# Kernel tuning notes

Measured on AMD Instinct MI355X. Metric: run time of the kernel, lower is better.

The kernel has to match this reference:

```python
import jax, jax.numpy as jnp
import numpy as np

T, D, N, K, H, F = 2048, 4096, 32, 8, 128, 14336
THETA = 500000.0
EPS = 1e-5


def setup_inputs() -> dict:
    key = jax.random.key(0)
    ks = jax.random.split(key, 10)
    s = 0.02  # weight init scale
    return {
        "x": jax.random.normal(ks[0], (T, D), jnp.float32),
        "positions": jnp.arange(T, dtype=jnp.int32),
        "ln1_scale": jnp.ones((D,), jnp.float32),
        "w_q": jax.random.normal(ks[1], (D, N, H), jnp.float32) * s,
        "w_k": jax.random.normal(ks[2], (D, K, H), jnp.float32) * s,
        "w_v": jax.random.normal(ks[3], (D, K, H), jnp.float32) * s,
        "w_o": jax.random.normal(ks[4], (N, H, D), jnp.float32) * s,
        "ln2_scale": jnp.ones((D,), jnp.float32),
        "w_gate": jax.random.normal(ks[5], (D, F), jnp.float32) * s,
        "w_up": jax.random.normal(ks[6], (D, F), jnp.float32) * s,
        "w_down": jax.random.normal(ks[7], (F, D), jnp.float32) * s,
    }


def _rms_norm(x, scale):
    var = jnp.mean(jnp.square(x), axis=-1, keepdims=True)
    return x * jax.lax.rsqrt(var + EPS) * scale


def _apply_rope(x, pos):
    # x: [T, heads, H]; Llama rotate-half RoPE
    half = H // 2
    inv_freq = 1.0 / (THETA ** (jnp.arange(half, dtype=jnp.float32) / half))
    ang = pos.astype(jnp.float32)[:, None] * inv_freq[None, :]      # [T, half]
    cos = jnp.cos(ang)[:, None, :]
    sin = jnp.sin(ang)[:, None, :]
    x1, x2 = x[..., :half], x[..., half:]
    return jnp.concatenate([x1 * cos - x2 * sin, x2 * cos + x1 * sin], axis=-1)


def reference(x, positions, ln1_scale, w_q, w_k, w_v, w_o, ln2_scale, w_gate, w_up, w_down):
    # --- input RMSNorm ---
    h = _rms_norm(x, ln1_scale)
    # --- QKV projections + RoPE ---
    q = _apply_rope(jnp.einsum('td,dnh->tnh', h, w_q), positions)   # [T,N,H]
    k = _apply_rope(jnp.einsum('td,dkh->tkh', h, w_k), positions)   # [T,K,H]
    v = jnp.einsum('td,dkh->tkh', h, w_v)                            # [T,K,H]
    # --- GQA causal attention (prefill) ---
    G = N // K
    qg = q.reshape(T, K, G, H)
    scale = 1.0 / jnp.sqrt(jnp.float32(H))
    scores = jnp.einsum('tkgh,skh->kgts', qg, k) * scale             # [K,G,T,T]
    causal = positions[:, None] >= positions[None, :]                # [T,T]
    scores = jnp.where(causal[None, None], scores, jnp.finfo(scores.dtype).min)
    probs = jax.nn.softmax(scores, axis=-1)
    attn = jnp.einsum('kgts,skh->tkgh', probs, v).reshape(T, N, H)
    attn_out = jnp.einsum('tnh,nhd->td', attn, w_o)
    # --- residual ---
    residual = attn_out + x
    # --- post-attn RMSNorm + SwiGLU MLP ---
    h2 = _rms_norm(residual, ln2_scale)
    gate = jax.nn.silu(h2 @ w_gate)
    up = h2 @ w_up
    out = (gate * up) @ w_down
    return residual + out
```

## Files before the change

kernel.cpp:

```cpp
#include <hip/hip_runtime.h>

typedef __attribute__((ext_vector_type(8))) short bf16x8;
typedef __attribute__((ext_vector_type(4))) float f32x4;

constexpr int T = 2048;
constexpr int D = 4096;
constexpr int NQ = 32;
constexpr int NKV = 8;
constexpr int H = 128;
constexpr int F = 14336;
constexpr int NQKV = (NQ + 2 * NKV) * H;
constexpr int VOFF = (NQ + NKV) * H;

__device__ inline unsigned short f2bf(float f) {
  unsigned u = __float_as_uint(f);
  return (unsigned short)((u + 0x7FFFu + ((u >> 16) & 1u)) >> 16);
}

__device__ inline void gload_lds16(const void* g, void* l) {
  __builtin_amdgcn_global_load_lds((const __attribute__((address_space(1))) void*)g,
                                   (__attribute__((address_space(3))) void*)l, 16, 0, 0);
}

#define MFMA16(a, b, c) __builtin_amdgcn_mfma_f32_16x16x32_bf16(a, b, c, 0, 0, 0)

template <int MODE>
__global__ __launch_bounds__(256) void transpose_bf16(const float* __restrict__ in,
                                                      unsigned short* __restrict__ out,
                                                      int K, int N) {
  __shared__ float tile[64 * 65];
  const int kb = blockIdx.x * 64;
  const int nb = blockIdx.y * 64;
  const int tid = threadIdx.x;
  const int r = tid >> 2;
  const int c4 = tid & 3;
#pragma unroll
  for (int i = 0; i < 4; ++i) {
    float4 v = *(const float4*)(in + (size_t)(kb + r) * N + nb + c4 * 16 + i * 4);
    *(float4*)&tile[r * 65 + c4 * 16 + i * 4] = v;
  }
  __syncthreads();
  const int n = tid >> 2;
  const int kq = tid & 3;
  int nsrc = nb + n;
  int prow = (MODE == 0) ? nsrc : ((nsrc >> 4) * 32 + (nsrc & 15) + (MODE == 2 ? 16 : 0));
#pragma unroll
  for (int half = 0; half < 2; ++half) {
    ushort4 o0, o1;
    int k0 = kq * 16 + half * 8;
    o0.x = f2bf(tile[(k0 + 0) * 65 + n]);
    o0.y = f2bf(tile[(k0 + 1) * 65 + n]);
    o0.z = f2bf(tile[(k0 + 2) * 65 + n]);
    o0.w = f2bf(tile[(k0 + 3) * 65 + n]);
    o1.x = f2bf(tile[(k0 + 4) * 65 + n]);
    o1.y = f2bf(tile[(k0 + 5) * 65 + n]);
    o1.z = f2bf(tile[(k0 + 6) * 65 + n]);
    o1.w = f2bf(tile[(k0 + 7) * 65 + n]);
    unsigned short* op = out + (size_t)prow * K + kb + k0;
    *(ushort4*)(op + 0) = o0;
    *(ushort4*)(op + 4) = o1;
  }
}

__global__ __launch_bounds__(256) void rmsnorm_kernel(
    const float* __restrict__ in, const float* __restrict__ scale,
    unsigned short* __restrict__ out) {
  int row = blockIdx.x;
  const float4* xr = (const float4*)(in + (size_t)row * D);
  const float4* sr = (const float4*)scale;
  float4 vals[4];
  float ss = 0.f;
#pragma unroll
  for (int i = 0; i < 4; ++i) {
    float4 v = xr[threadIdx.x + i * 256];
    vals[i] = v;
    ss += v.x * v.x + v.y * v.y + v.z * v.z + v.w * v.w;
  }
#pragma unroll
  for (int off = 32; off; off >>= 1) ss += __shfl_xor(ss, off, 64);
  __shared__ float wsum[4];
  if ((threadIdx.x & 63) == 0) wsum[threadIdx.x >> 6] = ss;
  __syncthreads();
  float r = rsqrtf((wsum[0] + wsum[1] + wsum[2] + wsum[3]) * (1.f / D) + 1e-5f);
#pragma unroll
  for (int i = 0; i < 4; ++i) {
    int vi = threadIdx.x + i * 256;
    float4 v = vals[i];
    float4 s = sr[vi];
    ushort4 o;
    o.x = f2bf(v.x * r * s.x);
    o.y = f2bf(v.y * r * s.y);
    o.z = f2bf(v.z * r * s.z);
    o.w = f2bf(v.w * r * s.w);
    *(ushort4*)(out + (size_t)row * D + (size_t)vi * 4) = o;
  }
}

__global__ __launch_bounds__(256) void rmsnorm_add3(
    const float* __restrict__ a, const float* __restrict__ b,
    const float* __restrict__ c, const float* __restrict__ scale,
    float* __restrict__ residOut, unsigned short* __restrict__ out) {
  int row = blockIdx.x;
  const float4* ar = (const float4*)(a + (size_t)row * D);
  const float4* br = (const float4*)(b + (size_t)row * D);
  const float4* cr = (const float4*)(c + (size_t)row * D);
  const float4* sr = (const float4*)scale;
  float4* rr = (float4*)(residOut + (size_t)row * D);
  float4 vals[4];
  float ss = 0.f;
#pragma unroll
  for (int i = 0; i < 4; ++i) {
    int vi = threadIdx.x + i * 256;
    float4 va = ar[vi], vb = br[vi], vc = cr[vi];
    float4 v;
    v.x = va.x + vb.x + vc.x;
    v.y = va.y + vb.y + vc.y;
    v.z = va.z + vb.z + vc.z;
    v.w = va.w + vb.w + vc.w;
    vals[i] = v;
    ss += v.x * v.x + v.y * v.y + v.z * v.z + v.w * v.w;
  }
#pragma unroll
  for (int off = 32; off; off >>= 1) ss += __shfl_xor(ss, off, 64);
  __shared__ float wsum[4];
  if ((threadIdx.x & 63) == 0) wsum[threadIdx.x >> 6] = ss;
  __syncthreads();
  float r = rsqrtf((wsum[0] + wsum[1] + wsum[2] + wsum[3]) * (1.f / D) + 1e-5f);
#pragma unroll
  for (int i = 0; i < 4; ++i) {
    int vi = threadIdx.x + i * 256;
    float4 v = vals[i];
    rr[vi] = v;
    float4 s = sr[vi];
    ushort4 o;
    o.x = f2bf(v.x * r * s.x);
    o.y = f2bf(v.y * r * s.y);
    o.z = f2bf(v.z * r * s.z);
    o.w = f2bf(v.w * r * s.w);
    *(ushort4*)(out + (size_t)row * D + (size_t)vi * 4) = o;
  }
}

__global__ __launch_bounds__(256) void add3_kernel(const float* __restrict__ a,
                                                   const float* __restrict__ b,
                                                   const float* __restrict__ c,
                                                   float* __restrict__ o) {
  int i = blockIdx.x * 256 + threadIdx.x;
  float4 va = ((const float4*)a)[i];
  float4 vb = ((const float4*)b)[i];
  float4 vc = ((const float4*)c)[i];
  float4 vo;
  vo.x = va.x + vb.x + vc.x;
  vo.y = va.y + vb.y + vc.y;
  vo.z = va.z + vb.z + vc.z;
  vo.w = va.w + vb.w + vc.w;
  ((float4*)o)[i] = vo;
}

__global__ __launch_bounds__(256) void rope_table(const int* __restrict__ pos,
                                                  float* __restrict__ ctab,
                                                  float* __restrict__ stab) {
  int idx = blockIdx.x * 256 + threadIdx.x;
  int t = idx >> 6, i = idx & 63;
  float inv = exp2f(-(float)i * (log2f(500000.0f) / 64.0f));
  float ang = (float)pos[t] * inv;
  ctab[idx] = cosf(ang);
  stab[idx] = sinf(ang);
}

__global__ __launch_bounds__(256) void rope_bf16(const float* __restrict__ x,
                                                 const float* __restrict__ ctab,
                                                 const float* __restrict__ stab,
                                                 unsigned short* __restrict__ out,
                                                 int nheads, int row_stride, float scale) {
  int idx = blockIdx.x * 256 + threadIdx.x;
  int i = idx & 63;
  int tn = idx >> 6;
  int t = tn / nheads;
  int n = tn - t * nheads;
  float c = ctab[t * 64 + i], s = stab[t * 64 + i];
  const float* p = x + (size_t)t * row_stride + n * H;
  float x1 = p[i], x2 = p[i + 64];
  unsigned short* o = out + (size_t)tn * H;
  o[i] = f2bf((x1 * c - x2 * s) * scale);
  o[i + 64] = f2bf((x2 * c + x1 * s) * scale);
}

template <int EP>
__global__ __launch_bounds__(256) void gemm_bf(
    const unsigned short* __restrict__ A, const unsigned short* __restrict__ Bt0,
    float* __restrict__ outF, unsigned short* __restrict__ outB, int Kd, int Nd) {
  __shared__ unsigned short lA[128 * 32];
  __shared__ unsigned short lB0[128 * 32];

  const int tid = threadIdx.x;
  const int m0 = blockIdx.x * 128;
  const int n0 = blockIdx.y * 128;
  const int lane = tid & 63;
  const int wv = tid >> 6;

  f32x4 acc[4][4];
#pragma unroll
  for (int i = 0; i < 4; ++i)
#pragma unroll
    for (int j = 0; j < 4; ++j) acc[i][j] = (f32x4){0.f, 0.f, 0.f, 0.f};

  const int wr = (wv >> 1) * 64;
  const int wc = (wv & 1) * 64;
  const int k8 = (lane >> 4) * 8;
  const int rl = lane & 15;
  const int sidx0 = wv * 512 + lane * 8;

  for (int k0 = 0; k0 < Kd; k0 += 32) {
    __syncthreads();
#pragma unroll
    for (int it = 0; it < 2; ++it) {
      int idx = sidx0 + it * 2048;
      int row = idx >> 5, kk = idx & 31;
      int base = wv * 512 + it * 2048;
      gload_lds16(A + (size_t)(m0 + row) * Kd + k0 + kk, &lA[base]);
      gload_lds16(Bt0 + (size_t)(n0 + row) * Kd + k0 + kk, &lB0[base]);
    }
    asm volatile("s_waitcnt vmcnt(0)" ::: "memory");
    __syncthreads();

    bf16x8 af[4], bfr[4];
#pragma unroll
    for (int i = 0; i < 4; ++i)
      af[i] = *(const bf16x8*)&lA[(wr + i * 16 + rl) * 32 + k8];
#pragma unroll
    for (int j = 0; j < 4; ++j)
      bfr[j] = *(const bf16x8*)&lB0[(wc + j * 16 + rl) * 32 + k8];
#pragma unroll
    for (int i = 0; i < 4; ++i)
#pragma unroll
      for (int j = 0; j < 4; ++j)
        acc[i][j] = MFMA16(af[i], bfr[j], acc[i][j]);
  }

  const int rb = (lane >> 4) * 4;
#pragma unroll
  for (int i = 0; i < 4; ++i)
#pragma unroll
    for (int j = 0; j < 4; ++j) {
      int col = n0 + wc + j * 16 + rl;
      if (EP == 4 && n0 >= VOFF) {
        int row0 = m0 + wr + i * 16 + rb;
        ushort4 o;
        o.x = f2bf(acc[i][j][0]);
        o.y = f2bf(acc[i][j][1]);
        o.z = f2bf(acc[i][j][2]);
        o.w = f2bf(acc[i][j][3]);
        *(ushort4*)&outB[(size_t)(col - VOFF) * T + row0] = o;
      } else {
#pragma unroll
        for (int jj = 0; jj < 4; ++jj) {
          int row = m0 + wr + i * 16 + rb + jj;
          outF[(size_t)row * Nd + col] = acc[i][j][jj];
        }
      }
    }
}

template <int EP>
__global__ __launch_bounds__(512, 2) void gemm256(
    const unsigned short* __restrict__ A, const unsigned short* __restrict__ Bt,
    float* __restrict__ outF, float* __restrict__ outF2,
    unsigned short* __restrict__ outB, int Kd, int Nd, int Klen) {
  __shared__ unsigned short lds[65536];
  const int tid = threadIdx.x, lane = tid & 63, wv = tid >> 6;
  const int wm = wv >> 2, wn = wv & 3;
  const int rl = lane & 15, g = lane >> 4;
  const int kz = blockIdx.z;
  int raw = blockIdx.x + blockIdx.y * gridDim.x;
  int cpx = (gridDim.x * gridDim.y) >> 3;
  int sid = (raw & 7) * cpx + (raw >> 3);
  int brow = sid % gridDim.x;
  int bcol = sid / gridDim.x;
  const int m0 = brow * 256, n0 = bcol * 256;

  const int l8 = lane >> 3;
  const int scol = ((lane & 7) ^ l8) * 8;
  const int xr = (rl & 7) << 4;
  const int pc0 = (g * 16) ^ xr;
  const int pc1 = (64 + g * 16) ^ xr;

  const char* ldsc = (const char*)lds;
  const unsigned short* gA = A + (size_t)(m0 + wv * 8 + l8) * Kd + kz * Klen + scol;
  const unsigned short* gB = Bt + (size_t)(n0 + wv * 8 + l8) * Kd + kz * Klen + scol;

  f32x4 acc[8][4];
#pragma unroll
  for (int i = 0; i < 8; ++i)
#pragma unroll
    for (int j = 0; j < 4; ++j) acc[i][j] = (f32x4){0.f, 0.f, 0.f, 0.f};

  const int NT = Klen >> 6;

#define STAGE_AL(kt, l)                                                      \
  gload_lds16(gA + (size_t)(kt) * 64 + (size_t)(l) * 64 * Kd,                \
              (void*)&lds[((kt) & 1) * 32768 + (l) * 4096 + wv * 512]);
#define STAGE_BL(kt, l)                                                      \
  gload_lds16(gB + (size_t)(kt) * 64 + (size_t)(l) * 64 * Kd,                \
              (void*)&lds[((kt) & 1) * 32768 + 16384 + (l) * 4096 + wv * 512]);
#define SBAR()                        \
  __builtin_amdgcn_sched_barrier(0);  \
  __builtin_amdgcn_s_barrier();

  STAGE_AL(0, 0); STAGE_AL(0, 1); STAGE_AL(0, 2); STAGE_AL(0, 3);
  STAGE_BL(0, 0); STAGE_BL(0, 1); STAGE_BL(0, 2); STAGE_BL(0, 3);
  STAGE_AL(1, 0); STAGE_AL(1, 1); STAGE_AL(1, 2); STAGE_AL(1, 3);
  STAGE_BL(1, 0); STAGE_BL(1, 1); STAGE_BL(1, 2); STAGE_BL(1, 3);
  asm volatile("s_waitcnt vmcnt(8)" ::: "memory");
  SBAR();

  const int bhalf = (wn >> 1) * 16384;
  const int brl = (wn & 1) * 64;

  bf16x8 bLoC[2][2];
  {
    const char* bB0 = ldsc + 32768 + bhalf;
#pragma unroll
    for (int nf = 0; nf < 2; ++nf) {
      bLoC[nf][0] = *(const bf16x8*)(bB0 + (brl + nf * 16 + rl) * 128 + pc0);
      bLoC[nf][1] = *(const bf16x8*)(bB0 + (brl + nf * 16 + rl) * 128 + pc1);
    }
  }

  for (int kt = 0; kt < NT; ++kt) {
    const int b = kt & 1;
    const char* aB = ldsc + b * 65536 + wm * 16384;
    const char* bB = ldsc + b * 65536 + 32768 + bhalf;
    const char* bBn = ldsc + (b ^ 1) * 65536 + 32768 + bhalf;
    const bool pre = (kt + 2 < NT);
    bf16x8 aLo[4][2], aHi[4][2], bHi[2][2], bLoN[2][2];
#pragma unroll
    for (int mf = 0; mf < 4; ++mf) {
      aLo[mf][0] = *(const bf16x8*)(aB + (mf * 16 + rl) * 128 + pc0);
      aLo[mf][1] = *(const bf16x8*)(aB + (mf * 16 + rl) * 128 + pc1);
    }
    SBAR();
    __builtin_amdgcn_s_setprio(1);
#pragma unroll
    for (int mf = 0; mf < 4; ++mf)
#pragma unroll
      for (int nf = 0; nf < 2; ++nf) {
        acc[mf][nf] = MFMA16(aLo[mf][0], bLoC[nf][0], acc[mf][nf]);
        acc[mf][nf] = MFMA16(aLo[mf][1], bLoC[nf][1], acc[mf][nf]);
      }
    __builtin_amdgcn_s_setprio(0);
    SBAR();
#pragma unroll
    for (int nf = 0; nf < 2; ++nf) {
      bHi[nf][0] = *(const bf16x8*)(bB + (brl + (nf + 2) * 16 + rl) * 128 + pc0);
      bHi[nf][1] = *(const bf16x8*)(bB + (brl + (nf + 2) * 16 + rl) * 128 + pc1);
    }
    if (pre) { STAGE_AL(kt + 2, 0); STAGE_AL(kt + 2, 2); }
    SBAR();
    __builtin_amdgcn_s_setprio(1);
#pragma unroll
    for (int mf = 0; mf < 4; ++mf)
#pragma unroll
      for (int nf = 0; nf < 2; ++nf) {
        acc[mf][nf + 2] = MFMA16(aLo[mf][0], bHi[nf][0], acc[mf][nf + 2]);
        acc[mf][nf + 2] = MFMA16(aLo[mf][1], bHi[nf][1], acc[mf][nf + 2]);
      }
    __builtin_amdgcn_s_setprio(0);
    SBAR();
#pragma unroll
    for (int mf = 0; mf < 4; ++mf) {
      aHi[mf][0] = *(const bf16x8*)(aB + ((mf + 4) * 16 + rl) * 128 + pc0);
      aHi[mf][1] = *(const bf16x8*)(aB + ((mf + 4) * 16 + rl) * 128 + pc1);
    }
    if (pre) {
      STAGE_BL(kt + 2, 0); STAGE_BL(kt + 2, 1);
      STAGE_BL(kt + 2, 2); STAGE_BL(kt + 2, 3);
      asm volatile("s_waitcnt vmcnt(6)" ::: "memory");
    } else {
      asm volatile("s_waitcnt vmcnt(0)" ::: "memory");
    }
    SBAR();
    __builtin_amdgcn_s_setprio(1);
#pragma unroll
    for (int mf = 0; mf < 4; ++mf)
#pragma unroll
      for (int nf = 0; nf < 2; ++nf) {
        acc[mf + 4][nf + 2] = MFMA16(aHi[mf][0], bHi[nf][0], acc[mf + 4][nf + 2]);
        acc[mf + 4][nf + 2] = MFMA16(aHi[mf][1], bHi[nf][1], acc[mf + 4][nf + 2]);
      }
    __builtin_amdgcn_s_setprio(0);
    SBAR();
    if (pre) { STAGE_AL(kt + 2, 1); STAGE_AL(kt + 2, 3); }
    if (kt + 1 < NT) {
#pragma unroll
      for (int nf = 0; nf < 2; ++nf) {
        bLoN[nf][0] = *(const bf16x8*)(bBn + (brl + nf * 16 + rl) * 128 + pc0);
        bLoN[nf][1] = *(const bf16x8*)(bBn + (brl + nf * 16 + rl) * 128 + pc1);
      }
    }
    SBAR();
    __builtin_amdgcn_s_setprio(1);
#pragma unroll
    for (int mf = 0; mf < 4; ++mf)
#pragma unroll
      for (int nf = 0; nf < 2; ++nf) {
        acc[mf + 4][nf] = MFMA16(aHi[mf][0], bLoC[nf][0], acc[mf + 4][nf]);
        acc[mf + 4][nf] = MFMA16(aHi[mf][1], bLoC[nf][1], acc[mf + 4][nf]);
      }
    __builtin_amdgcn_s_setprio(0);
    SBAR();
    if (kt + 1 < NT) {
#pragma unroll
      for (int nf = 0; nf < 2; ++nf) {
        bLoC[nf][0] = bLoN[nf][0];
        bLoC[nf][1] = bLoN[nf][1];
      }
    }
  }

  const int g4 = g * 4;
  if constexpr (EP == 5) {
    const int acolBase = ((n0 + wn * 64) >> 1) + rl;
#pragma unroll
    for (int mf = 0; mf < 8; ++mf)
#pragma unroll
      for (int p = 0; p < 2; ++p) {
        int acol = acolBase + p * 16;
#pragma unroll
        for (int jj = 0; jj < 4; ++jj) {
          int row = m0 + wm * 128 + mf * 16 + g4 + jj;
          float gg = acc[mf][2 * p][jj];
          float uu = acc[mf][2 * p + 1][jj];
          outB[(size_t)row * F + acol] = f2bf(gg / (1.f + __expf(-gg)) * uu);
        }
      }
  } else {
    float* dst = kz ? outF2 : outF;
#pragma unroll
    for (int mf = 0; mf < 8; ++mf)
#pragma unroll
      for (int q = 0; q < 4; ++q) {
        int col = n0 + wn * 64 + q * 16 + rl;
#pragma unroll
        for (int jj = 0; jj < 4; ++jj) {
          int row = m0 + wm * 128 + mf * 16 + g4 + jj;
          dst[(size_t)row * Nd + col] = acc[mf][q][jj];
        }
      }
  }
#undef STAGE_AL
#undef STAGE_BL
#undef SBAR
}

constexpr int KLD = 136;
constexpr int VLD = 72;
constexpr int PLD = 72;

__global__ __launch_bounds__(512) void flash_attn(
    const unsigned short* __restrict__ qbf, const unsigned short* __restrict__ kbf,
    const unsigned short* __restrict__ vtbf, unsigned short* __restrict__ out) {
  __shared__ unsigned short K_lds[64 * KLD];
  __shared__ unsigned short Vt_lds[H * VLD];
  __shared__ unsigned short P_lds[8 * 16 * PLD];

  const int tid = threadIdx.x;
  const int lane = tid & 63;
  const int wv = tid >> 6;
  const int qb = blockIdx.x;
  const int kvh = blockIdx.y;
  const int qh = wv & 3, rh = wv >> 2;
  const int n = kvh * 4 + qh;
  const int g = lane >> 4;
  const int rl = lane & 15;
  const int qrow = qb * 32 + rh * 16;

  bf16x8 qfrag[4];
  {
    const unsigned short* qp = qbf + ((size_t)(qrow + rl) * NQ + n) * H + g * 8;
#pragma unroll
    for (int ks = 0; ks < 4; ++ks) qfrag[ks] = *(const bf16x8*)(qp + ks * 32);
  }

  f32x4 oacc[8];
#pragma unroll
  for (int ob = 0; ob < 8; ++ob) oacc[ob] = (f32x4){0.f, 0.f, 0.f, 0.f};
  float mrun[4] = {-1e30f, -1e30f, -1e30f, -1e30f};
  float lrun[4] = {0.f, 0.f, 0.f, 0.f};

  const int krow = tid >> 3, kseg = (tid & 7) * 16;
  const int vh = tid >> 2, vseg = (tid & 3) * 16;

  const int ktmax = (qb * 32 + 31) >> 6;
  for (int kt = 0; kt <= ktmax; ++kt) {
    const int kbase = kt * 64;
    __syncthreads();
    {
      const unsigned short* kp = kbf + ((size_t)(kbase + krow) * NKV + kvh) * H + kseg;
      *(bf16x8*)&K_lds[krow * KLD + kseg] = *(const bf16x8*)kp;
      *(bf16x8*)&K_lds[krow * KLD + kseg + 8] = *(const bf16x8*)(kp + 8);
      const unsigned short* vp = vtbf + (size_t)(kvh * H + vh) * T + kbase + vseg;
      *(bf16x8*)&Vt_lds[vh * VLD + vseg] = *(const bf16x8*)vp;
      *(bf16x8*)&Vt_lds[vh * VLD + vseg + 8] = *(const bf16x8*)(vp + 8);
    }
    __syncthreads();

    f32x4 sacc[4];
#pragma unroll
    for (int cb = 0; cb < 4; ++cb) sacc[cb] = (f32x4){0.f, 0.f, 0.f, 0.f};
#pragma unroll
    for (int cb = 0; cb < 4; ++cb)
#pragma unroll
      for (int ks = 0; ks < 4; ++ks) {
        bf16x8 kf = *(const bf16x8*)&K_lds[(cb * 16 + rl) * KLD + ks * 32 + g * 8];
        sacc[cb] = MFMA16(qfrag[ks], kf, sacc[cb]);
      }

    if (kt == ktmax) {
#pragma unroll
      for (int cb = 0; cb < 4; ++cb) {
        int kv_abs = kbase + cb * 16 + rl;
#pragma unroll
        for (int r = 0; r < 4; ++r) {
          if (kv_abs > qrow + g * 4 + r) sacc[cb][r] = -1e30f;
        }
      }
    }

    float mx[4], sm[4], corr[4];
#pragma unroll
    for (int r = 0; r < 4; ++r) {
      float m0 = fmaxf(fmaxf(sacc[0][r], sacc[1][r]), fmaxf(sacc[2][r], sacc[3][r]));
#pragma unroll
      for (int off = 1; off < 16; off <<= 1) m0 = fmaxf(m0, __shfl_xor(m0, off, 64));
      float nm = fmaxf(mrun[r], m0);
      corr[r] = __expf(mrun[r] - nm);
      mrun[r] = nm;
      mx[r] = nm;
    }
#pragma unroll
    for (int cb = 0; cb < 4; ++cb)
#pragma unroll
      for (int r = 0; r < 4; ++r) sacc[cb][r] = __expf(sacc[cb][r] - mx[r]);
#pragma unroll
    for (int r = 0; r < 4; ++r) {
      float s0 = sacc[0][r] + sacc[1][r] + sacc[2][r] + sacc[3][r];
#pragma unroll
      for (int off = 1; off < 16; off <<= 1) s0 += __shfl_xor(s0, off, 64);
      sm[r] = s0;
      lrun[r] = lrun[r] * corr[r] + sm[r];
    }
#pragma unroll
    for (int ob = 0; ob < 8; ++ob)
#pragma unroll
      for (int r = 0; r < 4; ++r) oacc[ob][r] *= corr[r];

#pragma unroll
    for (int cb = 0; cb < 4; ++cb)
#pragma unroll
      for (int r = 0; r < 4; ++r)
        P_lds[(wv * 16 + g * 4 + r) * PLD + cb * 16 + rl] = f2bf(sacc[cb][r]);

    bf16x8 pa[2];
#pragma unroll
    for (int ks = 0; ks < 2; ++ks)
      pa[ks] = *(const bf16x8*)&P_lds[(wv * 16 + rl) * PLD + ks * 32 + g * 8];

#pragma unroll
    for (int ob = 0; ob < 8; ++ob)
#pragma unroll
      for (int ks = 0; ks < 2; ++ks) {
        bf16x8 vf = *(const bf16x8*)&Vt_lds[(ob * 16 + rl) * VLD + ks * 32 + g * 8];
        oacc[ob] = MFMA16(pa[ks], vf, oacc[ob]);
      }
  }

  float inv[4];
#pragma unroll
  for (int r = 0; r < 4; ++r) inv[r] = 1.f / lrun[r];
#pragma unroll
  for (int ob = 0; ob < 8; ++ob)
#pragma unroll
    for (int r = 0; r < 4; ++r) {
      int t = qrow + g * 4 + r;
      out[((size_t)t * NQ + n) * H + ob * 16 + rl] = f2bf(oacc[ob][r] * inv[r]);
    }
}

extern "C" void kernel_launch(void* const* d_in, const int* in_sizes, int n_in,
                              void* d_out, int out_size, void* d_ws, size_t ws_size,
                              hipStream_t stream) {
  (void)in_sizes; (void)n_in; (void)out_size; (void)ws_size;
  const float* x = (const float*)d_in[0];
  const int* positions = (const int*)d_in[1];
  const float* ln1 = (const float*)d_in[2];
  const float* w_q = (const float*)d_in[3];
  const float* w_k = (const float*)d_in[4];
  const float* w_v = (const float*)d_in[5];
  const float* w_o = (const float*)d_in[6];
  const float* ln2 = (const float*)d_in[7];
  const float* w_gate = (const float*)d_in[8];
  const float* w_up = (const float*)d_in[9];
  const float* w_down = (const float*)d_in[10];
  float* out = (float*)d_out;

  char* ws = (char*)d_ws;
  size_t off = 0;
  auto alloc = [&](size_t bytes) {
    char* p = ws + off;
    off += (bytes + 255) & ~(size_t)255;
    return p;
  };
  unsigned short* h_bf = (unsigned short*)alloc((size_t)T * D * 2);
  unsigned short* h2_bf = (unsigned short*)alloc((size_t)T * D * 2);
  unsigned short* attn_bf = (unsigned short*)alloc((size_t)T * NQ * H * 2);
  unsigned short* act_bf = (unsigned short*)alloc((size_t)T * F * 2);
  float* qkvf = (float*)alloc((size_t)T * NQKV * 4);
  float* resid = (float*)alloc((size_t)T * D * 4);
  float* ctab = (float*)alloc((size_t)T * 64 * 4);
  float* stab = (float*)alloc((size_t)T * 64 * 4);
  unsigned short* qbf = (unsigned short*)alloc((size_t)T * NQ * H * 2);
  unsigned short* kbf = (unsigned short*)alloc((size_t)T * NKV * H * 2);
  unsigned short* vtbf = (unsigned short*)alloc((size_t)NKV * H * T * 2);
  unsigned short* wqkvt = (unsigned short*)alloc((size_t)NQKV * D * 2);
  unsigned short* wot = (unsigned short*)alloc((size_t)D * NQ * H * 2);
  unsigned short* wgut = (unsigned short*)alloc((size_t)2 * F * D * 2);
  unsigned short* wdt = (unsigned short*)alloc((size_t)D * F * 2);
  float* part0 = qkvf;
  float* part1 = (float*)wqkvt;

  transpose_bf16<0><<<dim3(D / 64, (NQ * H) / 64), 256, 0, stream>>>(w_q, wqkvt, D, NQ * H);
  transpose_bf16<0><<<dim3(D / 64, (NKV * H) / 64), 256, 0, stream>>>(
      w_k, wqkvt + (size_t)NQ * H * D, D, NKV * H);
  transpose_bf16<0><<<dim3(D / 64, (NKV * H) / 64), 256, 0, stream>>>(
      w_v, wqkvt + (size_t)VOFF * D, D, NKV * H);
  transpose_bf16<0><<<dim3((NQ * H) / 64, D / 64), 256, 0, stream>>>(w_o, wot, NQ * H, D);
  transpose_bf16<1><<<dim3(D / 64, F / 64), 256, 0, stream>>>(w_gate, wgut, D, F);
  transpose_bf16<2><<<dim3(D / 64, F / 64), 256, 0, stream>>>(w_up, wgut, D, F);
  transpose_bf16<0><<<dim3(F / 64, D / 64), 256, 0, stream>>>(w_down, wdt, F, D);

  rmsnorm_kernel<<<T, 256, 0, stream>>>(x, ln1, h_bf);
  rope_table<<<(T * 64) / 256, 256, 0, stream>>>(positions, ctab, stab);
  gemm_bf<4><<<dim3(T / 128, NQKV / 128), 256, 0, stream>>>(
      h_bf, wqkvt, qkvf, vtbf, D, NQKV);
  rope_bf16<<<(T * NQ * 64) / 256, 256, 0, stream>>>(qkvf, ctab, stab, qbf, NQ, NQKV,
                                                     0.08838834764831845f);
  rope_bf16<<<(T * NKV * 64) / 256, 256, 0, stream>>>(qkvf + NQ * H, ctab, stab, kbf,
                                                      NKV, NQKV, 1.0f);
  flash_attn<<<dim3(T / 32, NKV), 512, 0, stream>>>(qbf, kbf, vtbf, attn_bf);
  gemm256<0><<<dim3(T / 256, D / 256, 2), 512, 0, stream>>>(
      attn_bf, wot, part0, part1, nullptr, NQ * H, D, NQ * H / 2);
  rmsnorm_add3<<<T, 256, 0, stream>>>(part0, part1, x, ln2, resid, h2_bf);
  gemm256<5><<<dim3(T / 256, (2 * F) / 256), 512, 0, stream>>>(
      h2_bf, wgut, nullptr, nullptr, act_bf, D, 2 * F, D);
  gemm256<0><<<dim3(T / 256, D / 256, 2), 512, 0, stream>>>(
      act_bf, wdt, part0, part1, nullptr, F, D, F / 2);
  add3_kernel<<<(T * D / 4) / 256, 256, 0, stream>>>(part0, part1, resid, out);
}
```

Measured before the change: 1.378 ms.

## Route QKV projection through pipelined 256-tile GEMM and drop intra-iteration barriers

Replaces the simple 128x128 single-buffered QKV GEMM with the double-buffered 256x256 gemm256 kernel, adding an EP==4 epilogue that writes V transposed in bf16 and Q/K in fp32. It also removes four block barriers between MFMA phases inside the gemm256 main loop, which affects every GEMM that uses it. The larger tile and software pipelining are meant to raise MFMA utilisation on the QKV projection. The QKV grid becomes much smaller (8x24 blocks), which may underfill the device. Removing the barriers risks LDS races between staged prefetch writes and fragment reads.

```diff
diff --git a/kernel.cpp b/kernel.cpp
--- a/kernel.cpp
+++ b/kernel.cpp
@@ -187,82 +187,6 @@
 }
 
 template <int EP>
-__global__ __launch_bounds__(256) void gemm_bf(
-    const unsigned short* __restrict__ A, const unsigned short* __restrict__ Bt0,
-    float* __restrict__ outF, unsigned short* __restrict__ outB, int Kd, int Nd) {
-  __shared__ unsigned short lA[128 * 32];
-  __shared__ unsigned short lB0[128 * 32];
-
-  const int tid = threadIdx.x;
-  const int m0 = blockIdx.x * 128;
-  const int n0 = blockIdx.y * 128;
-  const int lane = tid & 63;
-  const int wv = tid >> 6;
-
-  f32x4 acc[4][4];
-#pragma unroll
-  for (int i = 0; i < 4; ++i)
-#pragma unroll
-    for (int j = 0; j < 4; ++j) acc[i][j] = (f32x4){0.f, 0.f, 0.f, 0.f};
-
-  const int wr = (wv >> 1) * 64;
-  const int wc = (wv & 1) * 64;
-  const int k8 = (lane >> 4) * 8;
-  const int rl = lane & 15;
-  const int sidx0 = wv * 512 + lane * 8;
-
-  for (int k0 = 0; k0 < Kd; k0 += 32) {
-    __syncthreads();
-#pragma unroll
-    for (int it = 0; it < 2; ++it) {
-      int idx = sidx0 + it * 2048;
-      int row = idx >> 5, kk = idx & 31;
-      int base = wv * 512 + it * 2048;
-      gload_lds16(A + (size_t)(m0 + row) * Kd + k0 + kk, &lA[base]);
-      gload_lds16(Bt0 + (size_t)(n0 + row) * Kd + k0 + kk, &lB0[base]);
-    }
-    asm volatile("s_waitcnt vmcnt(0)" ::: "memory");
-    __syncthreads();
-
-    bf16x8 af[4], bfr[4];
-#pragma unroll
-    for (int i = 0; i < 4; ++i)
-      af[i] = *(const bf16x8*)&lA[(wr + i * 16 + rl) * 32 + k8];
-#pragma unroll
-    for (int j = 0; j < 4; ++j)
-      bfr[j] = *(const bf16x8*)&lB0[(wc + j * 16 + rl) * 32 + k8];
-#pragma unroll
-    for (int i = 0; i < 4; ++i)
-#pragma unroll
-      for (int j = 0; j < 4; ++j)
-        acc[i][j] = MFMA16(af[i], bfr[j], acc[i][j]);
-  }
-
-  const int rb = (lane >> 4) * 4;
-#pragma unroll
-  for (int i = 0; i < 4; ++i)
-#pragma unroll
-    for (int j = 0; j < 4; ++j) {
-      int col = n0 + wc + j * 16 + rl;
-      if (EP == 4 && n0 >= VOFF) {
-        int row0 = m0 + wr + i * 16 + rb;
-        ushort4 o;
-        o.x = f2bf(acc[i][j][0]);
-        o.y = f2bf(acc[i][j][1]);
-        o.z = f2bf(acc[i][j][2]);
-        o.w = f2bf(acc[i][j][3]);
-        *(ushort4*)&outB[(size_t)(col - VOFF) * T + row0] = o;
-      } else {
-#pragma unroll
-        for (int jj = 0; jj < 4; ++jj) {
-          int row = m0 + wr + i * 16 + rb + jj;
-          outF[(size_t)row * Nd + col] = acc[i][j][jj];
-        }
-      }
-    }
-}
-
-template <int EP>
 __global__ __launch_bounds__(512, 2) void gemm256(
     const unsigned short* __restrict__ A, const unsigned short* __restrict__ Bt,
     float* __restrict__ outF, float* __restrict__ outF2,
@@ -349,7 +273,6 @@
         acc[mf][nf] = MFMA16(aLo[mf][1], bLoC[nf][1], acc[mf][nf]);
       }
     __builtin_amdgcn_s_setprio(0);
-    SBAR();
 #pragma unroll
     for (int nf = 0; nf < 2; ++nf) {
       bHi[nf][0] = *(const bf16x8*)(bB + (brl + (nf + 2) * 16 + rl) * 128 + pc0);
@@ -366,7 +289,6 @@
         acc[mf][nf + 2] = MFMA16(aLo[mf][1], bHi[nf][1], acc[mf][nf + 2]);
       }
     __builtin_amdgcn_s_setprio(0);
-    SBAR();
 #pragma unroll
     for (int mf = 0; mf < 4; ++mf) {
       aHi[mf][0] = *(const bf16x8*)(aB + ((mf + 4) * 16 + rl) * 128 + pc0);
@@ -389,7 +311,6 @@
         acc[mf + 4][nf + 2] = MFMA16(aHi[mf][1], bHi[nf][1], acc[mf + 4][nf + 2]);
       }
     __builtin_amdgcn_s_setprio(0);
-    SBAR();
     if (pre) { STAGE_AL(kt + 2, 1); STAGE_AL(kt + 2, 3); }
     if (kt + 1 < NT) {
 #pragma unroll
@@ -408,7 +329,6 @@
         acc[mf + 4][nf] = MFMA16(aHi[mf][1], bLoC[nf][1], acc[mf + 4][nf]);
       }
     __builtin_amdgcn_s_setprio(0);
-    SBAR();
     if (kt + 1 < NT) {
 #pragma unroll
       for (int nf = 0; nf < 2; ++nf) {
@@ -434,6 +354,34 @@
           outB[(size_t)row * F + acol] = f2bf(gg / (1.f + __expf(-gg)) * uu);
         }
       }
+  } else if constexpr (EP == 4) {
+    if (n0 >= VOFF) {
+#pragma unroll
+      for (int mf = 0; mf < 8; ++mf)
+#pragma unroll
+        for (int q = 0; q < 4; ++q) {
+          int col = n0 + wn * 64 + q * 16 + rl;
+          int row0 = m0 + wm * 128 + mf * 16 + g4;
+          ushort4 o;
+          o.x = f2bf(acc[mf][q][0]);
+          o.y = f2bf(acc[mf][q][1]);
+          o.z = f2bf(acc[mf][q][2]);
+          o.w = f2bf(acc[mf][q][3]);
+          *(ushort4*)&outB[(size_t)(col - VOFF) * T + row0] = o;
+        }
+    } else {
+#pragma unroll
+      for (int mf = 0; mf < 8; ++mf)
+#pragma unroll
+        for (int q = 0; q < 4; ++q) {
+          int col = n0 + wn * 64 + q * 16 + rl;
+#pragma unroll
+          for (int jj = 0; jj < 4; ++jj) {
+            int row = m0 + wm * 128 + mf * 16 + g4 + jj;
+            outF[(size_t)row * Nd + col] = acc[mf][q][jj];
+          }
+        }
+    }
   } else {
     float* dst = kz ? outF2 : outF;
 #pragma unroll
@@ -641,8 +589,8 @@
 
   rmsnorm_kernel<<<T, 256, 0, stream>>>(x, ln1, h_bf);
   rope_table<<<(T * 64) / 256, 256, 0, stream>>>(positions, ctab, stab);
-  gemm_bf<4><<<dim3(T / 128, NQKV / 128), 256, 0, stream>>>(
-      h_bf, wqkvt, qkvf, vtbf, D, NQKV);
+  gemm256<4><<<dim3(T / 256, NQKV / 256, 1), 512, 0, stream>>>(
+      h_bf, wqkvt, qkvf, nullptr, vtbf, D, NQKV, D);
   rope_bf16<<<(T * NQ * 64) / 256, 256, 0, stream>>>(qkvf, ctab, stab, qbf, NQ, NQKV,
                                                      0.08838834764831845f);
   rope_bf16<<<(T * NKV * 64) / 256, 256, 0, stream>>>(qkvf + NQ * H, ctab, stab, kbf,
```

Result: faster. 1.283 ms (-6.9%).
